# Optimization experiments

Hardware: AMD Instinct MI355X
Metric: run time of the kernel (lower is better)

Reference implementation:

```python
import jax, jax.numpy as jnp
import numpy as np


def _shift_lr(t):
    # t: [B, L, H] -> (left, right) neighbor states with zero padding
    B, L, H = t.shape
    pad = jnp.zeros((B, 1, H), dtype=t.dtype)
    left = jnp.concatenate([pad, t[:, :-1, :]], axis=1)
    right = jnp.concatenate([t[:, 1:, :], pad], axis=1)
    return left, right


def setup_inputs() -> dict:
    key = jax.random.key(0)
    ks = jax.random.split(key, 7)
    B, L, H = 32, 2048, 256
    h_t = jax.random.normal(ks[0], (B, L, H), dtype=jnp.float32)
    x = jax.random.normal(ks[1], (B, L, H), dtype=jnp.float32)
    h_slot = jax.random.normal(ks[2], (B, L, H), dtype=jnp.float32)
    h_intent = jax.random.normal(ks[3], (B, L, H), dtype=jnp.float32)
    c_t = jax.random.normal(ks[4], (B, L, H), dtype=jnp.float32)
    # gate order: [i, o, f, l, r, u]; linear in = 6H, out = H
    Ws = jax.random.normal(ks[5], (6, 6 * H, H), dtype=jnp.float32) * 0.02
    bs = jnp.zeros((6, H), dtype=jnp.float32)
    return {"h_t": h_t, "x": x, "h_slot": h_slot, "h_intent": h_intent,
            "c_t": c_t, "Ws": Ws, "bs": bs}


def reference(h_t, x, h_slot, h_intent, c_t, Ws, bs):
    h_left, h_right = _shift_lr(h_t)
    # concat order: [h_mid, h_left, h_right, x, h_slot, h_intent] -> [B,L,6H]
    cat = jnp.concatenate([h_t, h_left, h_right, x, h_slot, h_intent], axis=-1)
    # one batched GEMM for all six gates: [6, B, L, H]
    gates = jnp.einsum('blc,gch->gblh', cat, Ws) + bs[:, None, None, :]
    i_t = jax.nn.sigmoid(gates[0])
    o_t = jax.nn.sigmoid(gates[1])
    f_t = jax.nn.sigmoid(gates[2])
    l_t = jax.nn.sigmoid(gates[3])
    r_t = jax.nn.sigmoid(gates[4])
    u_t = jnp.tanh(gates[5])
    # softmax across the 4 gates (axis 0 of the stack)
    soft = jax.nn.softmax(jnp.stack([i_t, f_t, l_t, r_t], axis=0), axis=0)
    i_t, f_t, l_t, r_t = soft[0], soft[1], soft[2], soft[3]
    c_left, c_right = _shift_lr(c_t)
    c_new = f_t * c_t + l_t * c_left + r_t * c_right + i_t * u_t
    h_new = o_t * jnp.tanh(c_new)
    return (h_new, c_new)
```

## Files before the change

### kernel.cpp

```cpp
#include <hip/hip_runtime.h>

typedef __attribute__((ext_vector_type(8))) short short8;
typedef __attribute__((ext_vector_type(4))) float f32x4;

#define BB 32
#define LL 2048
#define HH 256
#define MTOT (BB*LL)
#define KK 1536
#define HSIZE (MTOT*HH)

__device__ __forceinline__ unsigned short f2bf(float f){
    unsigned u = __builtin_bit_cast(unsigned, f);
    u += 0x7FFFu + ((u >> 16) & 1u);
    return (unsigned short)(u >> 16);
}
__device__ __forceinline__ unsigned pk2(float lo, float hi){
    return (unsigned)f2bf(lo) | ((unsigned)f2bf(hi) << 16);
}
__device__ __forceinline__ float sigm(float v){
    return 1.0f / (1.0f + __expf(-v));
}
__device__ __forceinline__ float ftanh(float v){
    v = fminf(fmaxf(v, -30.0f), 30.0f);
    float e = __expf(2.0f * v);
    return (e - 1.0f) / (e + 1.0f);
}

__global__ __launch_bounds__(256) void prep_bt(const float* __restrict__ Ws,
                                               unsigned short* __restrict__ Bt){
    __shared__ float tile[64][65];
    int bid = blockIdx.x;
    int kb = bid % 24; int tmp = bid / 24; int hb = tmp & 3; int g = tmp >> 2;
    int t = threadIdx.x;
    const float* src = Ws + (size_t)g * (KK * HH) + (size_t)(kb * 64) * HH + hb * 64;
    #pragma unroll
    for (int it = 0; it < 16; ++it){
        int e = it * 256 + t; int kk = e >> 6, hh = e & 63;
        tile[kk][hh] = src[(size_t)kk * HH + hh];
    }
    __syncthreads();
    unsigned short* dst = Bt + (size_t)(g * 256 + hb * 64) * KK + kb * 64;
    #pragma unroll
    for (int it = 0; it < 16; ++it){
        int e = it * 256 + t; int hh = e >> 6, kk = e & 63;
        dst[(size_t)hh * KK + kk] = f2bf(tile[kk][hh]);
    }
}

__global__ __launch_bounds__(512, 2) void slstm_fused(
    const float* __restrict__ h_t, const float* __restrict__ x,
    const float* __restrict__ h_slot, const float* __restrict__ h_intent,
    const float* __restrict__ c_t, const float* __restrict__ bs,
    const unsigned short* __restrict__ Bt, float* __restrict__ out)
{
    __shared__ unsigned short As[128 * 40];
    __shared__ unsigned short Bs[384 * 40];

    const int t    = threadIdx.x;
    const int wv   = t >> 6,  ln  = t & 63;
    const int rg   = wv >> 2, ht  = wv & 3;
    const int quad = ln >> 4, l16 = ln & 15;

    const int h_chunk = blockIdx.x & 3;
    const int m_block = blockIdx.x >> 2;
    const int h0      = h_chunk * 64;

    const int  arow = t >> 2;
    const int  akq  = (t & 3) << 3;
    const long mg   = (long)m_block * 128 + arow;
    const int  lseq = (int)(mg & (LL - 1));

    f32x4 acc[4][6] = {};

    for (int ks = 0; ks < 48; ++ks){
        {
            int c  = ks >> 3;
            int kk = ((ks & 7) << 5) + akq;
            const float* src; int sh;
            switch (c){
                case 0:  src = h_t;      sh =  0; break;
                case 1:  src = h_t;      sh = -1; break;
                case 2:  src = h_t;      sh =  1; break;
                case 3:  src = x;        sh =  0; break;
                case 4:  src = h_slot;   sh =  0; break;
                default: src = h_intent; sh =  0; break;
            }
            int sl = lseq + sh;
            float4 v0 = make_float4(0.f,0.f,0.f,0.f), v1 = v0;
            if ((unsigned)sl < (unsigned)LL){
                const float* p = src + ((mg + sh) * HH + kk);
                v0 = *(const float4*)p;
                v1 = *(const float4*)(p + 4);
            }
            uint4 w;
            w.x = pk2(v0.x, v0.y); w.y = pk2(v0.z, v0.w);
            w.z = pk2(v1.x, v1.y); w.w = pk2(v1.z, v1.w);
            *(uint4*)&As[arow * 40 + akq] = w;
        }
        #pragma unroll
        for (int i = 0; i < 3; ++i){
            int s   = i * 512 + t;
            int col = s >> 2;
            int kq  = (s & 3) << 3;
            int g   = col >> 6, hc = col & 63;
            const uint4 bv = *(const uint4*)(Bt + (size_t)(g * 256 + h0 + hc) * KK + ks * 32 + kq);
            *(uint4*)&Bs[col * 40 + kq] = bv;
        }
        __syncthreads();
        short8 a[4];
        #pragma unroll
        for (int mt = 0; mt < 4; ++mt)
            a[mt] = *(const short8*)&As[(rg * 64 + mt * 16 + l16) * 40 + quad * 8];
        #pragma unroll
        for (int g = 0; g < 6; ++g){
            short8 bfrag = *(const short8*)&Bs[(g * 64 + ht * 16 + l16) * 40 + quad * 8];
            #pragma unroll
            for (int mt = 0; mt < 4; ++mt)
                acc[mt][g] = __builtin_amdgcn_mfma_f32_16x16x32_bf16(a[mt], bfrag, acc[mt][g], 0, 0, 0);
        }
        __syncthreads();
    }

    const int h = h0 + ht * 16 + l16;
    float bias[6];
    #pragma unroll
    for (int g = 0; g < 6; ++g) bias[g] = bs[g * HH + h];

    #pragma unroll
    for (int mt = 0; mt < 4; ++mt){
        #pragma unroll
        for (int r = 0; r < 4; ++r){
            long row = (long)m_block * 128 + rg * 64 + mt * 16 + quad * 4 + r;
            int  ls  = (int)(row & (LL - 1));
            float gi = sigm(acc[mt][0][r] + bias[0]);
            float go = sigm(acc[mt][1][r] + bias[1]);
            float gf = sigm(acc[mt][2][r] + bias[2]);
            float gl = sigm(acc[mt][3][r] + bias[3]);
            float gr = sigm(acc[mt][4][r] + bias[4]);
            float gu = ftanh(acc[mt][5][r] + bias[5]);
            float ei = __expf(gi), ef = __expf(gf), el = __expf(gl), er = __expf(gr);
            float inv = 1.0f / (ei + ef + el + er);
            float cm  = c_t[row * HH + h];
            float clv = (ls > 0)      ? c_t[(row - 1) * HH + h] : 0.0f;
            float crv = (ls < LL - 1) ? c_t[(row + 1) * HH + h] : 0.0f;
            float cn  = (ef * cm + el * clv + er * crv + ei * gu) * inv;
            float hn  = go * ftanh(cn);
            out[row * HH + h]         = hn;
            out[HSIZE + row * HH + h] = cn;
        }
    }
}

extern "C" void kernel_launch(void* const* d_in, const int* in_sizes, int n_in,
                              void* d_out, int out_size, void* d_ws, size_t ws_size,
                              hipStream_t stream){
    const float* h_t      = (const float*)d_in[0];
    const float* x        = (const float*)d_in[1];
    const float* h_slot   = (const float*)d_in[2];
    const float* h_intent = (const float*)d_in[3];
    const float* c_t      = (const float*)d_in[4];
    const float* Ws       = (const float*)d_in[5];
    const float* bs       = (const float*)d_in[6];
    unsigned short* Bt    = (unsigned short*)d_ws;

    prep_bt<<<576, 256, 0, stream>>>(Ws, Bt);
    slstm_fused<<<2048, 512, 0, stream>>>(h_t, x, h_slot, h_intent, c_t, bs, Bt, (float*)d_out);
}
```

Baseline: 993.9 us.

## Drop LDS staging and load MFMA fragments directly from global memory

Removes the shared-memory tiles and barriers and has each lane load its A and B MFMA fragments straight from global memory. A new conversion pass writes h_t to bf16 so its three shifted uses read half the bytes. The other inputs are converted to bf16 in registers. The aim is to drop LDS round-trips and syncthreads. The risk is that B-fragment and A-row reuse across waves now depends on the L1/L2 caches instead of LDS, which may raise global traffic and make loads less coalesced.

```diff
diff --git a/kernel.cpp b/kernel.cpp
--- a/kernel.cpp
+++ b/kernel.cpp
@@ -27,6 +27,17 @@
     return (e - 1.0f) / (e + 1.0f);
 }
 
+__global__ __launch_bounds__(256) void conv_bf16(const float* __restrict__ src,
+                                                 unsigned short* __restrict__ dst){
+    int idx = blockIdx.x * 256 + threadIdx.x;
+    const float4* s = (const float4*)src;
+    float4 v0 = s[2 * idx], v1 = s[2 * idx + 1];
+    uint4 w;
+    w.x = pk2(v0.x, v0.y); w.y = pk2(v0.z, v0.w);
+    w.z = pk2(v1.x, v1.y); w.w = pk2(v1.z, v1.w);
+    ((uint4*)dst)[idx] = w;
+}
+
 __global__ __launch_bounds__(256) void prep_bt(const float* __restrict__ Ws,
                                                unsigned short* __restrict__ Bt){
     __shared__ float tile[64][65];
@@ -49,14 +60,12 @@
 }
 
 __global__ __launch_bounds__(512, 2) void slstm_fused(
-    const float* __restrict__ h_t, const float* __restrict__ x,
-    const float* __restrict__ h_slot, const float* __restrict__ h_intent,
-    const float* __restrict__ c_t, const float* __restrict__ bs,
-    const unsigned short* __restrict__ Bt, float* __restrict__ out)
+    const unsigned short* __restrict__ hb,
+    const float* __restrict__ x, const float* __restrict__ h_slot,
+    const float* __restrict__ h_intent, const float* __restrict__ c_t,
+    const float* __restrict__ bs, const unsigned short* __restrict__ Bt,
+    float* __restrict__ out)
 {
-    __shared__ unsigned short As[128 * 40];
-    __shared__ unsigned short Bs[384 * 40];
-
     const int t    = threadIdx.x;
     const int wv   = t >> 6,  ln  = t & 63;
     const int rg   = wv >> 2, ht  = wv & 3;
@@ -66,60 +75,75 @@
     const int m_block = blockIdx.x >> 2;
     const int h0      = h_chunk * 64;
 
-    const int  arow = t >> 2;
-    const int  akq  = (t & 3) << 3;
-    const long mg   = (long)m_block * 128 + arow;
-    const int  lseq = (int)(mg & (LL - 1));
+    long row[4]; int ls[4];
+    #pragma unroll
+    for (int mt = 0; mt < 4; ++mt){
+        row[mt] = (long)m_block * 128 + rg * 64 + mt * 16 + l16;
+        ls[mt]  = (int)(row[mt] & (LL - 1));
+    }
+
+    const unsigned short* bp = Bt + (size_t)(h0 + ht * 16 + l16) * KK + quad * 8;
 
     f32x4 acc[4][6] = {};
 
-    for (int ks = 0; ks < 48; ++ks){
-        {
-            int c  = ks >> 3;
-            int kk = ((ks & 7) << 5) + akq;
-            const float* src; int sh;
-            switch (c){
-                case 0:  src = h_t;      sh =  0; break;
-                case 1:  src = h_t;      sh = -1; break;
-                case 2:  src = h_t;      sh =  1; break;
-                case 3:  src = x;        sh =  0; break;
-                case 4:  src = h_slot;   sh =  0; break;
-                default: src = h_intent; sh =  0; break;
+    #pragma unroll
+    for (int c = 0; c < 3; ++c){
+        const int sh = (c == 0) ? 0 : ((c == 1) ? -1 : 1);
+        const unsigned short* ap[4]; bool va[4];
+        #pragma unroll
+        for (int mt = 0; mt < 4; ++mt){
+            va[mt] = ((unsigned)(ls[mt] + sh) < (unsigned)LL);
+            long r2 = va[mt] ? (row[mt] + sh) : row[mt];
+            ap[mt] = hb + r2 * HH + quad * 8;
+        }
+        #pragma unroll 2
+        for (int k8 = 0; k8 < 8; ++k8){
+            const int kk = k8 * 32;
+            short8 a[4];
+            #pragma unroll
+            for (int mt = 0; mt < 4; ++mt){
+                short8 v = *(const short8*)(ap[mt] + kk);
+                short8 z = {};
+                a[mt] = va[mt] ? v : z;
             }
-            int sl = lseq + sh;
-            float4 v0 = make_float4(0.f,0.f,0.f,0.f), v1 = v0;
-            if ((unsigned)sl < (unsigned)LL){
-                const float* p = src + ((mg + sh) * HH + kk);
-                v0 = *(const float4*)p;
-                v1 = *(const float4*)(p + 4);
+            #pragma unroll
+            for (int g = 0; g < 6; ++g){
+                short8 b = *(const short8*)(bp + (size_t)g * HH * KK + c * HH + kk);
+                #pragma unroll
+                for (int mt = 0; mt < 4; ++mt)
+                    acc[mt][g] = __builtin_amdgcn_mfma_f32_16x16x32_bf16(a[mt], b, acc[mt][g], 0, 0, 0);
             }
-            uint4 w;
-            w.x = pk2(v0.x, v0.y); w.y = pk2(v0.z, v0.w);
-            w.z = pk2(v1.x, v1.y); w.w = pk2(v1.z, v1.w);
-            *(uint4*)&As[arow * 40 + akq] = w;
         }
-        #pragma unroll
-        for (int i = 0; i < 3; ++i){
-            int s   = i * 512 + t;
-            int col = s >> 2;
-            int kq  = (s & 3) << 3;
-            int g   = col >> 6, hc = col & 63;
-            const uint4 bv = *(const uint4*)(Bt + (size_t)(g * 256 + h0 + hc) * KK + ks * 32 + kq);
-            *(uint4*)&Bs[col * 40 + kq] = bv;
-        }
-        __syncthreads();
-        short8 a[4];
+    }
+
+    const float* fsrc[3] = {x, h_slot, h_intent};
+    #pragma unroll
+    for (int c3 = 0; c3 < 3; ++c3){
+        const float* ap[4];
         #pragma unroll
         for (int mt = 0; mt < 4; ++mt)
-            a[mt] = *(const short8*)&As[(rg * 64 + mt * 16 + l16) * 40 + quad * 8];
-        #pragma unroll
-        for (int g = 0; g < 6; ++g){
-            short8 bfrag = *(const short8*)&Bs[(g * 64 + ht * 16 + l16) * 40 + quad * 8];
+            ap[mt] = fsrc[c3] + row[mt] * HH + quad * 8;
+        #pragma unroll 2
+        for (int k8 = 0; k8 < 8; ++k8){
+            const int kk = k8 * 32;
+            short8 a[4];
             #pragma unroll
-            for (int mt = 0; mt < 4; ++mt)
-                acc[mt][g] = __builtin_amdgcn_mfma_f32_16x16x32_bf16(a[mt], bfrag, acc[mt][g], 0, 0, 0);
+            for (int mt = 0; mt < 4; ++mt){
+                float4 v0 = *(const float4*)(ap[mt] + kk);
+                float4 v1 = *(const float4*)(ap[mt] + kk + 4);
+                union { uint4 u; short8 s; } cv;
+                cv.u.x = pk2(v0.x, v0.y); cv.u.y = pk2(v0.z, v0.w);
+                cv.u.z = pk2(v1.x, v1.y); cv.u.w = pk2(v1.z, v1.w);
+                a[mt] = cv.s;
+            }
+            #pragma unroll
+            for (int g = 0; g < 6; ++g){
+                short8 b = *(const short8*)(bp + (size_t)g * HH * KK + (3 + c3) * HH + kk);
+                #pragma unroll
+                for (int mt = 0; mt < 4; ++mt)
+                    acc[mt][g] = __builtin_amdgcn_mfma_f32_16x16x32_bf16(a[mt], b, acc[mt][g], 0, 0, 0);
+            }
         }
-        __syncthreads();
     }
 
     const int h = h0 + ht * 16 + l16;
@@ -131,8 +155,8 @@
     for (int mt = 0; mt < 4; ++mt){
         #pragma unroll
         for (int r = 0; r < 4; ++r){
-            long row = (long)m_block * 128 + rg * 64 + mt * 16 + quad * 4 + r;
-            int  ls  = (int)(row & (LL - 1));
+            long orow = (long)m_block * 128 + rg * 64 + mt * 16 + quad * 4 + r;
+            int  lsq  = (int)(orow & (LL - 1));
             float gi = sigm(acc[mt][0][r] + bias[0]);
             float go = sigm(acc[mt][1][r] + bias[1]);
             float gf = sigm(acc[mt][2][r] + bias[2]);
@@ -141,13 +165,13 @@
             float gu = ftanh(acc[mt][5][r] + bias[5]);
             float ei = __expf(gi), ef = __expf(gf), el = __expf(gl), er = __expf(gr);
             float inv = 1.0f / (ei + ef + el + er);
-            float cm  = c_t[row * HH + h];
-            float clv = (ls > 0)      ? c_t[(row - 1) * HH + h] : 0.0f;
-            float crv = (ls < LL - 1) ? c_t[(row + 1) * HH + h] : 0.0f;
+            float cm  = c_t[orow * HH + h];
+            float clv = (lsq > 0)      ? c_t[(orow - 1) * HH + h] : 0.0f;
+            float crv = (lsq < LL - 1) ? c_t[(orow + 1) * HH + h] : 0.0f;
             float cn  = (ef * cm + el * clv + er * crv + ei * gu) * inv;
             float hn  = go * ftanh(cn);
-            out[row * HH + h]         = hn;
-            out[HSIZE + row * HH + h] = cn;
+            out[orow * HH + h]         = hn;
+            out[HSIZE + orow * HH + h] = cn;
         }
     }
 }
@@ -162,8 +186,11 @@
     const float* c_t      = (const float*)d_in[4];
     const float* Ws       = (const float*)d_in[5];
     const float* bs       = (const float*)d_in[6];
-    unsigned short* Bt    = (unsigned short*)d_ws;
 
+    unsigned short* Bt = (unsigned short*)d_ws;
+    unsigned short* hb = (unsigned short*)((char*)d_ws + (size_t)KK * KK * 2);
+
+    conv_bf16<<<8192, 256, 0, stream>>>(h_t, hb);
     prep_bt<<<576, 256, 0, stream>>>(Ws, Bt);
-    slstm_fused<<<2048, 512, 0, stream>>>(h_t, x, h_slot, h_intent, c_t, bs, Bt, (float*)d_out);
+    slstm_fused<<<2048, 512, 0, stream>>>(hb, x, h_slot, h_intent, c_t, bs, Bt, (float*)d_out);
 }
```

Result: slower. 1.508 ms (+51.7%).
